# Kernel tuning notes

Measured on AMD Instinct MI355X. Metric: run time of the kernel, lower is better.

The kernel has to match this reference:

```python
import jax, jax.numpy as jnp
import numpy as np

EPS = 1e-8


def box2corners(box):
    # box: (B,N,5) = x,y,w,h,alpha -> corners (B,N,4,2), CCW template
    x, y, w, h, alpha = (box[..., i] for i in range(5))
    tx = jnp.array([0.5, -0.5, -0.5, 0.5], dtype=box.dtype)
    ty = jnp.array([0.5, 0.5, -0.5, -0.5], dtype=box.dtype)
    x_off = w[..., None] * tx          # (B,N,4)
    y_off = h[..., None] * ty
    c = jnp.cos(alpha)[..., None]
    s = jnp.sin(alpha)[..., None]
    cx = x[..., None] + c * x_off - s * y_off
    cy = y[..., None] + s * x_off + c * y_off
    return jnp.stack([cx, cy], axis=-1)


def box_intersection(corners1, corners2):
    # all pairwise edge intersections: (B,N,4,4,2) points + (B,N,4,4) mask
    line1 = jnp.concatenate([corners1, jnp.roll(corners1, -1, axis=2)], axis=-1)
    line2 = jnp.concatenate([corners2, jnp.roll(corners2, -1, axis=2)], axis=-1)
    l1 = line1[:, :, :, None, :]   # (B,N,4,1,4)
    l2 = line2[:, :, None, :, :]   # (B,N,1,4,4)
    x1, y1, x2, y2 = (l1[..., i] for i in range(4))
    x3, y3, x4, y4 = (l2[..., i] for i in range(4))
    num = (y4 - y3) * (x2 - x1) - (x4 - x3) * (y2 - y1)
    den_t = (x4 - x3) * (y1 - y3) - (y4 - y3) * (x1 - x3)
    den_u = (x2 - x1) * (y1 - y3) - (y2 - y1) * (x1 - x3)
    safe = jnp.where(num == 0., 1., num)
    t = jnp.where(num == 0., -1., den_t / safe)
    u = jnp.where(num == 0., -1., -den_u / safe)
    mask = (t > 0.) & (t < 1.) & (u > 0.) & (u < 1.)
    px = x1 + t * (x2 - x1)
    py = y1 + t * (y2 - y1)
    pts = jnp.stack([px, py], axis=-1) * mask[..., None].astype(corners1.dtype)
    return pts, mask


def box1_in_box2(corners1, corners2):
    # which corners of box1 lie inside box2 -> (B,N,4) bool
    a = corners2[:, :, 0:1, :]
    b = corners2[:, :, 1:2, :]
    d = corners2[:, :, 3:4, :]
    ab, ad, am = b - a, d - a, corners1 - a
    p_ab = jnp.sum(ab * am, axis=-1)
    p_ad = jnp.sum(ad * am, axis=-1)
    n_ab = jnp.sum(ab * ab, axis=-1)
    n_ad = jnp.sum(ad * ad, axis=-1)
    eps = 1e-6
    c1 = (p_ab / n_ab > -eps) & (p_ab / n_ab < 1. + eps)
    c2 = (p_ad / n_ad > -eps) & (p_ad / n_ad < 1. + eps)
    return c1 & c2


def oriented_box_intersection_2d(corners1, corners2):
    # intersection area of two rotated boxes via vertex sort + shoelace
    inters, m_int = box_intersection(corners1, corners2)       # (B,N,4,4,2)
    c1_in_2 = box1_in_box2(corners1, corners2)                 # (B,N,4)
    c2_in_1 = box1_in_box2(corners2, corners1)
    B, N = corners1.shape[0], corners1.shape[1]
    verts = jnp.concatenate([corners1, corners2,
                             inters.reshape(B, N, 16, 2)], axis=2)  # (B,N,24,2)
    mask = jnp.concatenate([c1_in_2, c2_in_1,
                            m_int.reshape(B, N, 16)], axis=2)       # (B,N,24)
    maskf = mask.astype(verts.dtype)
    nv = jnp.sum(mask, axis=-1)                                # (B,N) int, num valid
    mean = (jnp.sum(verts * maskf[..., None], axis=2, keepdims=True)
            / jnp.maximum(nv[..., None, None].astype(verts.dtype), 1.))
    rel = verts - mean
    ang = jnp.where(mask, jnp.arctan2(rel[..., 1], rel[..., 0]), 1e6)
    order = jnp.argsort(ang, axis=-1)                          # valid CCW, invalid last
    sorted_v = jnp.take_along_axis(verts, order[..., None], axis=2)
    # pad invalid slots with first valid vertex: zero shoelace contribution
    sel = jnp.arange(24)[None, None, :] < nv[..., None]
    poly = jnp.where(sel[..., None], sorted_v, sorted_v[:, :, 0:1, :])
    nxt = jnp.roll(poly, -1, axis=2)
    area = 0.5 * jnp.abs(jnp.sum(poly[..., 0] * nxt[..., 1]
                                 - nxt[..., 0] * poly[..., 1], axis=-1))
    return area


def diff_iou_rotated_3d(box3d1, box3d2):
    # boxes: (B,N,7) = x,y,z,dx,dy,dz,yaw
    idx = jnp.array([0, 1, 3, 4, 6])
    c1 = box2corners(box3d1[..., idx])
    c2 = box2corners(box3d2[..., idx])
    inter_2d = oriented_box_intersection_2d(c1, c2)
    zmax1 = box3d1[..., 2] + box3d1[..., 5] * 0.5
    zmin1 = box3d1[..., 2] - box3d1[..., 5] * 0.5
    zmax2 = box3d2[..., 2] + box3d2[..., 5] * 0.5
    zmin2 = box3d2[..., 2] - box3d2[..., 5] * 0.5
    z_overlap = jnp.clip(jnp.minimum(zmax1, zmax2) - jnp.maximum(zmin1, zmin2), 0.)
    inter_3d = inter_2d * z_overlap
    v1 = box3d1[..., 3] * box3d1[..., 4] * box3d1[..., 5]
    v2 = box3d2[..., 3] * box3d2[..., 4] * box3d2[..., 5]
    union = v1 + v2 - inter_3d
    return inter_3d / union


def setup_inputs() -> dict:
    key = jax.random.key(0)
    k1, k2, k3, k4, k5 = jax.random.split(key, 5)
    N = 500000
    ctr = jax.random.uniform(k1, (N, 3), minval=-40., maxval=40.)
    dims = jax.random.uniform(k2, (N, 3), minval=1., maxval=5.)
    yaw = jax.random.uniform(k3, (N, 1), minval=-np.pi, maxval=np.pi)
    pred = jnp.concatenate([ctr, dims, yaw], axis=-1).astype(jnp.float32)
    noise = jax.random.normal(k4, (N, 7), dtype=jnp.float32) * jnp.array(
        [0.5, 0.5, 0.3, 0.3, 0.3, 0.3, 0.2], dtype=jnp.float32)
    target = pred + noise
    target = target.at[:, 3:6].set(jnp.maximum(target[:, 3:6], 0.5))
    weight = jax.random.uniform(k5, (N,), dtype=jnp.float32)
    return {"pred": pred, "target": target, "weight": weight}


def reference(pred, target, weight):
    loss_weight = 1.0
    target = jnp.where(jnp.isnan(target), pred, target)
    iou = diff_iou_rotated_3d(pred[None], target[None])        # (1,N)
    loss = 1. - iou
    loss = loss * weight[None]
    return loss_weight * jnp.mean(loss)
```

## Files before the change

### kernel.cpp

```cpp
#include <hip/hip_runtime.h>
#include <hip/hip_fp16.h>
#include <math.h>

#define THREADS 64
#define VSTRIDE 25

__device__ __forceinline__ float prcp(float x) { return __builtin_amdgcn_rcpf(x); }

__device__ __forceinline__ unsigned packh2(float x, float y) {
    __half2 h = __floats2half2_rn(x, y);
    return *reinterpret_cast<unsigned*>(&h);
}
__device__ __forceinline__ void unpackh2(unsigned u, float& x, float& y) {
    __half2 h = *reinterpret_cast<__half2*>(&u);
    x = __low2float(h); y = __high2float(h);
}

__global__ void __launch_bounds__(THREADS) iou3d_kernel(
    const float* __restrict__ pred, const float* __restrict__ tgt,
    const float* __restrict__ wgt, float* __restrict__ partial, int N) {
    __shared__ unsigned ldsbuf[THREADS * VSTRIDE];
    int tid = threadIdx.x;
    unsigned* myv = &ldsbuf[tid * VSTRIDE];
    int n = blockIdx.x * THREADS + tid;
    float loss = 0.0f;
    if (n < N) {
        float p[7], t[7];
#pragma unroll
        for (int k = 0; k < 7; k++) {
            p[k] = pred[(size_t)n * 7 + k];
            float tv = tgt[(size_t)n * 7 + k];
            t[k] = (tv != tv) ? p[k] : tv;
        }
        float w = wgt[n];
        float zmax1 = p[2] + p[5] * 0.5f, zmin1 = p[2] - p[5] * 0.5f;
        float zmax2 = t[2] + t[5] * 0.5f, zmin2 = t[2] - t[5] * 0.5f;
        float zov = fmaxf(fminf(zmax1, zmax2) - fmaxf(zmin1, zmin2), 0.0f);
        float vol1 = p[3] * p[4] * p[5], vol2 = t[3] * t[4] * t[5];

        float hw1 = 0.5f * p[3], hh1 = 0.5f * p[4];
        float hw2 = 0.5f * t[3], hh2 = 0.5f * t[4];
        float s1, c1v, s2, c2v;
        __sincosf(p[6], &s1, &c1v);
        __sincosf(t[6], &s2, &c2v);
        float c12 = c1v * c2v + s1 * s2;
        float s12 = s1 * c2v - c1v * s2;
        float ddx = p[0] - t[0], ddy = p[1] - t[1];
        float T12x =  c2v * ddx + s2 * ddy;
        float T12y = -s2 * ddx + c2v * ddy;
        float T21x = -(c1v * ddx + s1 * ddy);
        float T21y =  s1 * ddx - c1v * ddy;
        float ux = c12 * hw1, uy = s12 * hw1;
        float wx = -s12 * hh1, wy = c12 * hh1;
        float fx[4], fy[4];
        fx[0] = T12x + ux + wx; fy[0] = T12y + uy + wy;
        fx[1] = T12x - ux + wx; fy[1] = T12y - uy + wy;
        fx[2] = T12x - ux - wx; fy[2] = T12y - uy - wy;
        fx[3] = T12x + ux - wx; fy[3] = T12y + uy - wy;

        unsigned vm = 0;
        float bx2 = hw2 * (1.0f + 2e-6f), by2 = hh2 * (1.0f + 2e-6f);
#pragma unroll
        for (int k = 0; k < 4; k++) {
            bool c = (fabsf(fx[k]) < bx2) && (fabsf(fy[k]) < by2);
            vm |= ((unsigned)c) << k;
        }
        float u2x = c12 * hw2, u2y = -s12 * hw2;
        float v2x = s12 * hh2, v2y = c12 * hh2;
        float bx1 = hw1 * (1.0f + 2e-6f), by1 = hh1 * (1.0f + 2e-6f);
        {
            float qx, qy;
            qx = T21x + u2x + v2x; qy = T21y + u2y + v2y;
            vm |= ((unsigned)((fabsf(qx) < bx1) && (fabsf(qy) < by1))) << 4;
            qx = T21x - u2x + v2x; qy = T21y - u2y + v2y;
            vm |= ((unsigned)((fabsf(qx) < bx1) && (fabsf(qy) < by1))) << 5;
            qx = T21x - u2x - v2x; qy = T21y - u2y - v2y;
            vm |= ((unsigned)((fabsf(qx) < bx1) && (fabsf(qy) < by1))) << 6;
            qx = T21x + u2x - v2x; qy = T21y + u2y - v2y;
            vm |= ((unsigned)((fabsf(qx) < bx1) && (fabsf(qy) < by1))) << 7;
        }
        float sx = 0.0f, sy = 0.0f;
#pragma unroll
        for (int k = 0; k < 4; k++) {
            myv[k] = packh2(fx[k], fy[k]);
            bool v = (vm >> k) & 1u;
            sx += v ? fx[k] : 0.0f; sy += v ? fy[k] : 0.0f;
        }
        myv[4] = packh2(hw2, hh2);  myv[5] = packh2(-hw2, hh2);
        myv[6] = packh2(-hw2, -hh2); myv[7] = packh2(hw2, -hh2);
        {
            bool v4 = (vm >> 4) & 1u, v5 = (vm >> 5) & 1u, v6 = (vm >> 6) & 1u, v7 = (vm >> 7) & 1u;
            sx += (v4 ? hw2 : 0.0f) + (v5 ? -hw2 : 0.0f) + (v6 ? -hw2 : 0.0f) + (v7 ? hw2 : 0.0f);
            sy += (v4 ? hh2 : 0.0f) + (v5 ? hh2 : 0.0f) + (v6 ? -hh2 : 0.0f) + (v7 ? -hh2 : 0.0f);
        }

        float tux = ux + ux, tuy = uy + uy, twx = wx + wx, twy = wy + wy;
        float rtux = prcp(tux), rtuy = prcp(tuy), rtwx = prcp(twx), rtwy = prcp(twy);
        float dxe[4] = {-tux, -twx, tux, twx};
        float dye[4] = {-tuy, -twy, tuy, twy};
        float rdxe[4] = {-rtux, -rtwx, rtux, rtwx};
        float rdye[4] = {-rtuy, -rtwy, rtuy, rtwy};
        float r2w = prcp(hw2 + hw2), r2h = prcp(hh2 + hh2);

        float pvar[16];
#pragma unroll
        for (int e1 = 0; e1 < 4; e1++) {
            float x1 = fx[e1], y1 = fy[e1];
            {
                float tt = (hh2 - y1) * rdye[e1];
                float px = fmaf(tt, dxe[e1], x1);
                float uu = (hw2 - px) * (-r2w);
                bool mk = (tt > 0.0f) && (tt < 1.0f) && (uu > 0.0f) && (uu < 1.0f);
                pvar[e1 * 4 + 0] = px;
                float pxm = mk ? px : 0.0f, pym = mk ? hh2 : 0.0f;
                myv[8 + e1 * 4 + 0] = packh2(pxm, pym);
                sx += pxm; sy += pym;
                vm |= ((unsigned)mk) << (8 + e1 * 4 + 0);
            }
            {
                float tt = (-hw2 - x1) * rdxe[e1];
                float py = fmaf(tt, dye[e1], y1);
                float uu = (hh2 - py) * (-r2h);
                bool mk = (tt > 0.0f) && (tt < 1.0f) && (uu > 0.0f) && (uu < 1.0f);
                pvar[e1 * 4 + 1] = py;
                float pxm = mk ? -hw2 : 0.0f, pym = mk ? py : 0.0f;
                myv[8 + e1 * 4 + 1] = packh2(pxm, pym);
                sx += pxm; sy += pym;
                vm |= ((unsigned)mk) << (8 + e1 * 4 + 1);
            }
            {
                float tt = (-hh2 - y1) * rdye[e1];
                float px = fmaf(tt, dxe[e1], x1);
                float uu = (-hw2 - px) * r2w;
                bool mk = (tt > 0.0f) && (tt < 1.0f) && (uu > 0.0f) && (uu < 1.0f);
                pvar[e1 * 4 + 2] = px;
                float pxm = mk ? px : 0.0f, pym = mk ? -hh2 : 0.0f;
                myv[8 + e1 * 4 + 2] = packh2(pxm, pym);
                sx += pxm; sy += pym;
                vm |= ((unsigned)mk) << (8 + e1 * 4 + 2);
            }
            {
                float tt = (hw2 - x1) * rdxe[e1];
                float py = fmaf(tt, dye[e1], y1);
                float uu = (-hh2 - py) * r2h;
                bool mk = (tt > 0.0f) && (tt < 1.0f) && (uu > 0.0f) && (uu < 1.0f);
                pvar[e1 * 4 + 3] = py;
                float pxm = mk ? hw2 : 0.0f, pym = mk ? py : 0.0f;
                myv[8 + e1 * 4 + 3] = packh2(pxm, pym);
                sx += pxm; sy += pym;
                vm |= ((unsigned)mk) << (8 + e1 * 4 + 3);
            }
        }

        int nv = __popc(vm);
        float r0 = prcp(fmaxf((float)nv, 1.0f));
        float mx = sx * r0, my = sy * r0;

        unsigned ka[24];
#define MKKEY(K, XR, YR) do { \
        float xr_ = (XR), yr_ = (YR); \
        float d_ = fabsf(xr_) + fabsf(yr_); \
        float q_ = 1.0f - xr_ * prcp(d_); \
        float pa_ = copysignf(q_, yr_) + 4.0f; \
        unsigned key_ = (__float_as_uint(pa_) & 0xFFFFFFE0u) | (unsigned)(K); \
        ka[K] = ((vm >> (K)) & 1u) ? key_ : (0x7F000000u | (unsigned)(K)); \
    } while (0)
        float hpx = hw2 - mx, hmx = -hw2 - mx, hpy = hh2 - my, hmy = -hh2 - my;
#pragma unroll
        for (int k = 0; k < 4; k++) MKKEY(k, fx[k] - mx, fy[k] - my);
        MKKEY(4, hpx, hpy); MKKEY(5, hmx, hpy); MKKEY(6, hmx, hmy); MKKEY(7, hpx, hmy);
#pragma unroll
        for (int e1 = 0; e1 < 4; e1++) {
            MKKEY(8 + e1 * 4 + 0, pvar[e1 * 4 + 0] - mx, hpy);
            MKKEY(8 + e1 * 4 + 1, hmx, pvar[e1 * 4 + 1] - my);
            MKKEY(8 + e1 * 4 + 2, pvar[e1 * 4 + 2] - mx, hmy);
            MKKEY(8 + e1 * 4 + 3, hpx, pvar[e1 * 4 + 3] - my);
        }
#undef MKKEY

#define CE(A, B) { unsigned lo_ = ka[A] < ka[B] ? ka[A] : ka[B]; \
                   unsigned hi_ = ka[A] < ka[B] ? ka[B] : ka[A]; \
                   ka[A] = lo_; ka[B] = hi_; }
        CE(0,1); CE(2,3); CE(4,5); CE(6,7); CE(8,9); CE(10,11); CE(12,13); CE(14,15); CE(16,17); CE(18,19); CE(20,21); CE(22,23);
        CE(0,2); CE(1,3); CE(4,6); CE(5,7); CE(8,10); CE(9,11); CE(12,14); CE(13,15); CE(16,18); CE(17,19); CE(20,22); CE(21,23);
        CE(1,2); CE(5,6); CE(9,10); CE(13,14); CE(17,18); CE(21,22);
        CE(0,4); CE(1,5); CE(2,6); CE(3,7); CE(8,12); CE(9,13); CE(10,14); CE(11,15); CE(16,20); CE(17,21); CE(18,22); CE(19,23);
        CE(2,4); CE(3,5); CE(10,12); CE(11,13); CE(18,20); CE(19,21);
        CE(1,2); CE(3,4); CE(5,6); CE(9,10); CE(11,12); CE(13,14); CE(17,18); CE(19,20); CE(21,22);
        CE(0,8); CE(1,9); CE(2,10); CE(3,11); CE(4,12); CE(5,13); CE(6,14); CE(7,15);
        CE(4,8); CE(5,9); CE(6,10); CE(7,11);
        CE(2,4); CE(3,5); CE(6,8); CE(7,9); CE(10,12); CE(11,13); CE(18,20); CE(19,21);
        CE(1,2); CE(3,4); CE(5,6); CE(7,8); CE(9,10); CE(11,12); CE(13,14); CE(17,18); CE(19,20); CE(21,22);
        CE(0,16); CE(1,17); CE(2,18); CE(3,19); CE(4,20); CE(5,21); CE(6,22); CE(7,23);
        CE(8,16); CE(9,17); CE(10,18); CE(11,19); CE(12,20); CE(13,21); CE(14,22); CE(15,23);
        CE(4,8); CE(5,9); CE(6,10); CE(7,11); CE(12,16); CE(13,17); CE(14,18); CE(15,19);
        CE(2,4); CE(3,5); CE(6,8); CE(7,9); CE(10,12); CE(11,13); CE(14,16); CE(15,17); CE(18,20); CE(19,21);
        CE(1,2); CE(3,4); CE(5,6); CE(7,8); CE(9,10); CE(11,12); CE(13,14); CE(15,16); CE(17,18); CE(19,20); CE(21,22);
#undef CE

        unsigned gu[24];
#pragma unroll
        for (int i = 0; i < 24; i++) gu[i] = myv[ka[i] & 31u];
        float g0x, g0y;
        unpackh2(gu[0], g0x, g0y);
        float prevx = g0x, prevy = g0y;
        float area2 = 0.0f;
#pragma unroll
        for (int i = 1; i < 24; i++) {
            float xx, yy;
            unpackh2(gu[i], xx, yy);
            bool c = i < nv;
            float cxv = c ? xx : g0x;
            float cyv = c ? yy : g0y;
            area2 += prevx * cyv - cxv * prevy;
            prevx = cxv; prevy = cyv;
        }
        area2 += prevx * g0y - g0x * prevy;
        float inter2d = 0.5f * fabsf(area2);

        float inter3d = inter2d * zov;
        float uni = vol1 + vol2 - inter3d;
        float iou = inter3d / uni;
        loss = (1.0f - iou) * w;
    }

#pragma unroll
    for (int off = 32; off > 0; off >>= 1) loss += __shfl_down(loss, off, 64);
    if (threadIdx.x == 0) partial[blockIdx.x] = loss;
}

__global__ void __launch_bounds__(1024) reduce_kernel(const float* __restrict__ partial,
                                                      int nb, float* __restrict__ out, int N) {
    float s = 0.0f;
    for (int i = threadIdx.x; i < nb; i += 1024) s += partial[i];
#pragma unroll
    for (int off = 32; off > 0; off >>= 1) s += __shfl_down(s, off, 64);
    __shared__ float sm[16];
    int lane = threadIdx.x & 63, wv = threadIdx.x >> 6;
    if (lane == 0) sm[wv] = s;
    __syncthreads();
    if (threadIdx.x == 0) {
        float tot = 0.0f;
#pragma unroll
        for (int k = 0; k < 16; k++) tot += sm[k];
        out[0] = tot / (float)N;
    }
}

extern "C" void kernel_launch(void* const* d_in, const int* in_sizes, int n_in,
                              void* d_out, int out_size, void* d_ws, size_t ws_size,
                              hipStream_t stream) {
    const float* pred = (const float*)d_in[0];
    const float* tgt  = (const float*)d_in[1];
    const float* wgt  = (const float*)d_in[2];
    int N = in_sizes[2];
    int nb = (N + THREADS - 1) / THREADS;
    float* partial = (float*)d_ws;
    iou3d_kernel<<<nb, THREADS, 0, stream>>>(pred, tgt, wgt, partial, N);
    reduce_kernel<<<1, 1024, 0, stream>>>(partial, nb, (float*)d_out, N);
}
```

Measured before the change: 28.76 us.

## Process two boxes per thread with interleaved sorting networks and column-major LDS

Each thread now handles two box pairs and interleaves their 24-key sorting networks, giving the scheduler independent instructions to hide latency. The LDS vertex buffer is changed from a per-thread stride of 25 to a slot-major layout indexed by thread id, which changes the bank access pattern. The edge-intersection range test now compares the intersection coordinate against multiples of the half extents instead of multiplying by precomputed reciprocals, dropping two rcp operations. Register pressure roughly doubles and the grid is halved, which may reduce occupancy and the number of waves in flight.

```diff
diff --git a/kernel.cpp b/kernel.cpp
--- a/kernel.cpp
+++ b/kernel.cpp
@@ -3,7 +3,6 @@
 #include <math.h>
 
 #define THREADS 64
-#define VSTRIDE 25
 
 __device__ __forceinline__ float prcp(float x) { return __builtin_amdgcn_rcpf(x); }
 
@@ -19,27 +18,41 @@
 __global__ void __launch_bounds__(THREADS) iou3d_kernel(
     const float* __restrict__ pred, const float* __restrict__ tgt,
     const float* __restrict__ wgt, float* __restrict__ partial, int N) {
-    __shared__ unsigned ldsbuf[THREADS * VSTRIDE];
+    __shared__ unsigned ldsbuf[48 * THREADS];
     int tid = threadIdx.x;
-    unsigned* myv = &ldsbuf[tid * VSTRIDE];
-    int n = blockIdx.x * THREADS + tid;
+#define LDSV(Q, S) ldsbuf[((((Q) * 24) + (S)) << 6) + tid]
     float loss = 0.0f;
-    if (n < N) {
+
+    float zov[2], volsum[2], wgtv[2], hw2a[2], hh2a[2];
+    float fxa[2][4], fya[2][4];
+    float pv[2][16];
+    float sxa[2], sya[2];
+    unsigned vma[2];
+    int nva[2];
+    unsigned ka0[24], ka1[24];
+
+#pragma unroll
+    for (int q = 0; q < 2; q++) {
+        int n = blockIdx.x * (2 * THREADS) + tid + q * THREADS;
+        bool live = n < N;
+        int nc = live ? n : (N - 1);
         float p[7], t[7];
 #pragma unroll
         for (int k = 0; k < 7; k++) {
-            p[k] = pred[(size_t)n * 7 + k];
-            float tv = tgt[(size_t)n * 7 + k];
+            p[k] = pred[(size_t)nc * 7 + k];
+            float tv = tgt[(size_t)nc * 7 + k];
             t[k] = (tv != tv) ? p[k] : tv;
         }
-        float w = wgt[n];
+        wgtv[q] = live ? wgt[nc] : 0.0f;
+
         float zmax1 = p[2] + p[5] * 0.5f, zmin1 = p[2] - p[5] * 0.5f;
         float zmax2 = t[2] + t[5] * 0.5f, zmin2 = t[2] - t[5] * 0.5f;
-        float zov = fmaxf(fminf(zmax1, zmax2) - fmaxf(zmin1, zmin2), 0.0f);
-        float vol1 = p[3] * p[4] * p[5], vol2 = t[3] * t[4] * t[5];
+        zov[q] = fmaxf(fminf(zmax1, zmax2) - fmaxf(zmin1, zmin2), 0.0f);
+        volsum[q] = p[3] * p[4] * p[5] + t[3] * t[4] * t[5];
 
         float hw1 = 0.5f * p[3], hh1 = 0.5f * p[4];
         float hw2 = 0.5f * t[3], hh2 = 0.5f * t[4];
+        hw2a[q] = hw2; hh2a[q] = hh2;
         float s1, c1v, s2, c2v;
         __sincosf(p[6], &s1, &c1v);
         __sincosf(t[6], &s2, &c2v);
@@ -57,6 +70,8 @@
         fx[1] = T12x - ux + wx; fy[1] = T12y - uy + wy;
         fx[2] = T12x - ux - wx; fy[2] = T12y - uy - wy;
         fx[3] = T12x + ux - wx; fy[3] = T12y + uy - wy;
+#pragma unroll
+        for (int k = 0; k < 4; k++) { fxa[q][k] = fx[k]; fya[q][k] = fy[k]; }
 
         unsigned vm = 0;
         float bx2 = hw2 * (1.0f + 2e-6f), by2 = hh2 * (1.0f + 2e-6f);
@@ -82,12 +97,12 @@
         float sx = 0.0f, sy = 0.0f;
 #pragma unroll
         for (int k = 0; k < 4; k++) {
-            myv[k] = packh2(fx[k], fy[k]);
+            LDSV(q, k) = packh2(fx[k], fy[k]);
             bool v = (vm >> k) & 1u;
             sx += v ? fx[k] : 0.0f; sy += v ? fy[k] : 0.0f;
         }
-        myv[4] = packh2(hw2, hh2);  myv[5] = packh2(-hw2, hh2);
-        myv[6] = packh2(-hw2, -hh2); myv[7] = packh2(hw2, -hh2);
+        LDSV(q, 4) = packh2(hw2, hh2);   LDSV(q, 5) = packh2(-hw2, hh2);
+        LDSV(q, 6) = packh2(-hw2, -hh2); LDSV(q, 7) = packh2(hw2, -hh2);
         {
             bool v4 = (vm >> 4) & 1u, v5 = (vm >> 5) & 1u, v6 = (vm >> 6) & 1u, v7 = (vm >> 7) & 1u;
             sx += (v4 ? hw2 : 0.0f) + (v5 ? -hw2 : 0.0f) + (v6 ? -hw2 : 0.0f) + (v7 ? hw2 : 0.0f);
@@ -100,129 +115,138 @@
         float dye[4] = {-tuy, -twy, tuy, twy};
         float rdxe[4] = {-rtux, -rtwx, rtux, rtwx};
         float rdye[4] = {-rtuy, -rtwy, rtuy, rtwy};
-        float r2w = prcp(hw2 + hw2), r2h = prcp(hh2 + hh2);
-
-        float pvar[16];
+        float w3 = 3.0f * hw2, h3 = 3.0f * hh2;
 #pragma unroll
         for (int e1 = 0; e1 < 4; e1++) {
             float x1 = fx[e1], y1 = fy[e1];
             {
                 float tt = (hh2 - y1) * rdye[e1];
                 float px = fmaf(tt, dxe[e1], x1);
-                float uu = (hw2 - px) * (-r2w);
-                bool mk = (tt > 0.0f) && (tt < 1.0f) && (uu > 0.0f) && (uu < 1.0f);
-                pvar[e1 * 4 + 0] = px;
+                bool mk = (tt > 0.0f) && (tt < 1.0f) && (px > hw2) && (px < w3);
+                pv[q][e1 * 4 + 0] = px;
                 float pxm = mk ? px : 0.0f, pym = mk ? hh2 : 0.0f;
-                myv[8 + e1 * 4 + 0] = packh2(pxm, pym);
+                LDSV(q, 8 + e1 * 4 + 0) = packh2(pxm, pym);
                 sx += pxm; sy += pym;
                 vm |= ((unsigned)mk) << (8 + e1 * 4 + 0);
             }
             {
                 float tt = (-hw2 - x1) * rdxe[e1];
                 float py = fmaf(tt, dye[e1], y1);
-                float uu = (hh2 - py) * (-r2h);
-                bool mk = (tt > 0.0f) && (tt < 1.0f) && (uu > 0.0f) && (uu < 1.0f);
-                pvar[e1 * 4 + 1] = py;
+                bool mk = (tt > 0.0f) && (tt < 1.0f) && (py > hh2) && (py < h3);
+                pv[q][e1 * 4 + 1] = py;
                 float pxm = mk ? -hw2 : 0.0f, pym = mk ? py : 0.0f;
-                myv[8 + e1 * 4 + 1] = packh2(pxm, pym);
+                LDSV(q, 8 + e1 * 4 + 1) = packh2(pxm, pym);
                 sx += pxm; sy += pym;
                 vm |= ((unsigned)mk) << (8 + e1 * 4 + 1);
             }
             {
                 float tt = (-hh2 - y1) * rdye[e1];
                 float px = fmaf(tt, dxe[e1], x1);
-                float uu = (-hw2 - px) * r2w;
-                bool mk = (tt > 0.0f) && (tt < 1.0f) && (uu > 0.0f) && (uu < 1.0f);
-                pvar[e1 * 4 + 2] = px;
+                bool mk = (tt > 0.0f) && (tt < 1.0f) && (px < -hw2) && (px > -w3);
+                pv[q][e1 * 4 + 2] = px;
                 float pxm = mk ? px : 0.0f, pym = mk ? -hh2 : 0.0f;
-                myv[8 + e1 * 4 + 2] = packh2(pxm, pym);
+                LDSV(q, 8 + e1 * 4 + 2) = packh2(pxm, pym);
                 sx += pxm; sy += pym;
                 vm |= ((unsigned)mk) << (8 + e1 * 4 + 2);
             }
             {
                 float tt = (hw2 - x1) * rdxe[e1];
                 float py = fmaf(tt, dye[e1], y1);
-                float uu = (-hh2 - py) * r2h;
-                bool mk = (tt > 0.0f) && (tt < 1.0f) && (uu > 0.0f) && (uu < 1.0f);
-                pvar[e1 * 4 + 3] = py;
+                bool mk = (tt > 0.0f) && (tt < 1.0f) && (py < -hh2) && (py > -h3);
+                pv[q][e1 * 4 + 3] = py;
                 float pxm = mk ? hw2 : 0.0f, pym = mk ? py : 0.0f;
-                myv[8 + e1 * 4 + 3] = packh2(pxm, pym);
+                LDSV(q, 8 + e1 * 4 + 3) = packh2(pxm, pym);
                 sx += pxm; sy += pym;
                 vm |= ((unsigned)mk) << (8 + e1 * 4 + 3);
             }
         }
-
-        int nv = __popc(vm);
-        float r0 = prcp(fmaxf((float)nv, 1.0f));
-        float mx = sx * r0, my = sy * r0;
-
-        unsigned ka[24];
-#define MKKEY(K, XR, YR) do { \
+        vma[q] = vm; sxa[q] = sx; sya[q] = sy;
+    }
+
+#define KEYBUILD(Q, KA) do { \
+        unsigned vm = vma[Q]; \
+        int nv = __popc(vm); nva[Q] = nv; \
+        float r0 = prcp(fmaxf((float)nv, 1.0f)); \
+        float mx = sxa[Q] * r0, my = sya[Q] * r0; \
+        float hw2 = hw2a[Q], hh2 = hh2a[Q]; \
+        float hpx = hw2 - mx, hmx = -hw2 - mx, hpy = hh2 - my, hmy = -hh2 - my; \
+        MK(KA, 0, fxa[Q][0] - mx, fya[Q][0] - my); \
+        MK(KA, 1, fxa[Q][1] - mx, fya[Q][1] - my); \
+        MK(KA, 2, fxa[Q][2] - mx, fya[Q][2] - my); \
+        MK(KA, 3, fxa[Q][3] - mx, fya[Q][3] - my); \
+        MK(KA, 4, hpx, hpy); MK(KA, 5, hmx, hpy); MK(KA, 6, hmx, hmy); MK(KA, 7, hpx, hmy); \
+        MK(KA, 8,  pv[Q][0] - mx, hpy);  MK(KA, 9,  hmx, pv[Q][1] - my); \
+        MK(KA, 10, pv[Q][2] - mx, hmy);  MK(KA, 11, hpx, pv[Q][3] - my); \
+        MK(KA, 12, pv[Q][4] - mx, hpy);  MK(KA, 13, hmx, pv[Q][5] - my); \
+        MK(KA, 14, pv[Q][6] - mx, hmy);  MK(KA, 15, hpx, pv[Q][7] - my); \
+        MK(KA, 16, pv[Q][8] - mx, hpy);  MK(KA, 17, hmx, pv[Q][9] - my); \
+        MK(KA, 18, pv[Q][10] - mx, hmy); MK(KA, 19, hpx, pv[Q][11] - my); \
+        MK(KA, 20, pv[Q][12] - mx, hpy); MK(KA, 21, hmx, pv[Q][13] - my); \
+        MK(KA, 22, pv[Q][14] - mx, hmy); MK(KA, 23, hpx, pv[Q][15] - my); \
+    } while (0)
+#define MK(KA, K, XR, YR) do { \
         float xr_ = (XR), yr_ = (YR); \
         float d_ = fabsf(xr_) + fabsf(yr_); \
         float q_ = 1.0f - xr_ * prcp(d_); \
         float pa_ = copysignf(q_, yr_) + 4.0f; \
         unsigned key_ = (__float_as_uint(pa_) & 0xFFFFFFE0u) | (unsigned)(K); \
-        ka[K] = ((vm >> (K)) & 1u) ? key_ : (0x7F000000u | (unsigned)(K)); \
+        KA[K] = ((vm >> (K)) & 1u) ? key_ : (0x7F000000u | (unsigned)(K)); \
     } while (0)
-        float hpx = hw2 - mx, hmx = -hw2 - mx, hpy = hh2 - my, hmy = -hh2 - my;
-#pragma unroll
-        for (int k = 0; k < 4; k++) MKKEY(k, fx[k] - mx, fy[k] - my);
-        MKKEY(4, hpx, hpy); MKKEY(5, hmx, hpy); MKKEY(6, hmx, hmy); MKKEY(7, hpx, hmy);
-#pragma unroll
-        for (int e1 = 0; e1 < 4; e1++) {
-            MKKEY(8 + e1 * 4 + 0, pvar[e1 * 4 + 0] - mx, hpy);
-            MKKEY(8 + e1 * 4 + 1, hmx, pvar[e1 * 4 + 1] - my);
-            MKKEY(8 + e1 * 4 + 2, pvar[e1 * 4 + 2] - mx, hmy);
-            MKKEY(8 + e1 * 4 + 3, hpx, pvar[e1 * 4 + 3] - my);
-        }
-#undef MKKEY
-
-#define CE(A, B) { unsigned lo_ = ka[A] < ka[B] ? ka[A] : ka[B]; \
-                   unsigned hi_ = ka[A] < ka[B] ? ka[B] : ka[A]; \
-                   ka[A] = lo_; ka[B] = hi_; }
-        CE(0,1); CE(2,3); CE(4,5); CE(6,7); CE(8,9); CE(10,11); CE(12,13); CE(14,15); CE(16,17); CE(18,19); CE(20,21); CE(22,23);
-        CE(0,2); CE(1,3); CE(4,6); CE(5,7); CE(8,10); CE(9,11); CE(12,14); CE(13,15); CE(16,18); CE(17,19); CE(20,22); CE(21,23);
-        CE(1,2); CE(5,6); CE(9,10); CE(13,14); CE(17,18); CE(21,22);
-        CE(0,4); CE(1,5); CE(2,6); CE(3,7); CE(8,12); CE(9,13); CE(10,14); CE(11,15); CE(16,20); CE(17,21); CE(18,22); CE(19,23);
-        CE(2,4); CE(3,5); CE(10,12); CE(11,13); CE(18,20); CE(19,21);
-        CE(1,2); CE(3,4); CE(5,6); CE(9,10); CE(11,12); CE(13,14); CE(17,18); CE(19,20); CE(21,22);
-        CE(0,8); CE(1,9); CE(2,10); CE(3,11); CE(4,12); CE(5,13); CE(6,14); CE(7,15);
-        CE(4,8); CE(5,9); CE(6,10); CE(7,11);
-        CE(2,4); CE(3,5); CE(6,8); CE(7,9); CE(10,12); CE(11,13); CE(18,20); CE(19,21);
-        CE(1,2); CE(3,4); CE(5,6); CE(7,8); CE(9,10); CE(11,12); CE(13,14); CE(17,18); CE(19,20); CE(21,22);
-        CE(0,16); CE(1,17); CE(2,18); CE(3,19); CE(4,20); CE(5,21); CE(6,22); CE(7,23);
-        CE(8,16); CE(9,17); CE(10,18); CE(11,19); CE(12,20); CE(13,21); CE(14,22); CE(15,23);
-        CE(4,8); CE(5,9); CE(6,10); CE(7,11); CE(12,16); CE(13,17); CE(14,18); CE(15,19);
-        CE(2,4); CE(3,5); CE(6,8); CE(7,9); CE(10,12); CE(11,13); CE(14,16); CE(15,17); CE(18,20); CE(19,21);
-        CE(1,2); CE(3,4); CE(5,6); CE(7,8); CE(9,10); CE(11,12); CE(13,14); CE(15,16); CE(17,18); CE(19,20); CE(21,22);
+    KEYBUILD(0, ka0);
+    KEYBUILD(1, ka1);
+#undef MK
+#undef KEYBUILD
+
+#define CE1(KA, A, B) { unsigned lo_ = KA[A] < KA[B] ? KA[A] : KA[B]; \
+                        unsigned hi_ = KA[A] < KA[B] ? KA[B] : KA[A]; \
+                        KA[A] = lo_; KA[B] = hi_; }
+#define CE(A, B) CE1(ka0, A, B) CE1(ka1, A, B)
+    CE(0,1); CE(2,3); CE(4,5); CE(6,7); CE(8,9); CE(10,11); CE(12,13); CE(14,15); CE(16,17); CE(18,19); CE(20,21); CE(22,23);
+    CE(0,2); CE(1,3); CE(4,6); CE(5,7); CE(8,10); CE(9,11); CE(12,14); CE(13,15); CE(16,18); CE(17,19); CE(20,22); CE(21,23);
+    CE(1,2); CE(5,6); CE(9,10); CE(13,14); CE(17,18); CE(21,22);
+    CE(0,4); CE(1,5); CE(2,6); CE(3,7); CE(8,12); CE(9,13); CE(10,14); CE(11,15); CE(16,20); CE(17,21); CE(18,22); CE(19,23);
+    CE(2,4); CE(3,5); CE(10,12); CE(11,13); CE(18,20); CE(19,21);
+    CE(1,2); CE(3,4); CE(5,6); CE(9,10); CE(11,12); CE(13,14); CE(17,18); CE(19,20); CE(21,22);
+    CE(0,8); CE(1,9); CE(2,10); CE(3,11); CE(4,12); CE(5,13); CE(6,14); CE(7,15);
+    CE(4,8); CE(5,9); CE(6,10); CE(7,11);
+    CE(2,4); CE(3,5); CE(6,8); CE(7,9); CE(10,12); CE(11,13); CE(18,20); CE(19,21);
+    CE(1,2); CE(3,4); CE(5,6); CE(7,8); CE(9,10); CE(11,12); CE(13,14); CE(17,18); CE(19,20); CE(21,22);
+    CE(0,16); CE(1,17); CE(2,18); CE(3,19); CE(4,20); CE(5,21); CE(6,22); CE(7,23);
+    CE(8,16); CE(9,17); CE(10,18); CE(11,19); CE(12,20); CE(13,21); CE(14,22); CE(15,23);
+    CE(4,8); CE(5,9); CE(6,10); CE(7,11); CE(12,16); CE(13,17); CE(14,18); CE(15,19);
+    CE(2,4); CE(3,5); CE(6,8); CE(7,9); CE(10,12); CE(11,13); CE(14,16); CE(15,17); CE(18,20); CE(19,21);
+    CE(1,2); CE(3,4); CE(5,6); CE(7,8); CE(9,10); CE(11,12); CE(13,14); CE(15,16); CE(17,18); CE(19,20); CE(21,22);
 #undef CE
-
-        unsigned gu[24];
-#pragma unroll
-        for (int i = 0; i < 24; i++) gu[i] = myv[ka[i] & 31u];
-        float g0x, g0y;
-        unpackh2(gu[0], g0x, g0y);
-        float prevx = g0x, prevy = g0y;
-        float area2 = 0.0f;
-#pragma unroll
-        for (int i = 1; i < 24; i++) {
-            float xx, yy;
-            unpackh2(gu[i], xx, yy);
-            bool c = i < nv;
-            float cxv = c ? xx : g0x;
-            float cyv = c ? yy : g0y;
-            area2 += prevx * cyv - cxv * prevy;
-            prevx = cxv; prevy = cyv;
-        }
-        area2 += prevx * g0y - g0x * prevy;
-        float inter2d = 0.5f * fabsf(area2);
-
-        float inter3d = inter2d * zov;
-        float uni = vol1 + vol2 - inter3d;
-        float iou = inter3d / uni;
-        loss = (1.0f - iou) * w;
-    }
+#undef CE1
+
+#define SHOELACE(Q, KA) do { \
+        unsigned gu[24]; \
+        _Pragma("unroll") \
+        for (int i = 0; i < 24; i++) \
+            gu[i] = ldsbuf[((((Q) * 24) + (KA[i] & 31u)) << 6) + tid]; \
+        int nv = nva[Q]; \
+        float g0x, g0y; unpackh2(gu[0], g0x, g0y); \
+        float prevx = g0x, prevy = g0y, area2 = 0.0f; \
+        _Pragma("unroll") \
+        for (int i = 1; i < 24; i++) { \
+            float xx, yy; unpackh2(gu[i], xx, yy); \
+            bool c = i < nv; \
+            float cxv = c ? xx : g0x; \
+            float cyv = c ? yy : g0y; \
+            area2 += prevx * cyv - cxv * prevy; \
+            prevx = cxv; prevy = cyv; \
+        } \
+        area2 += prevx * g0y - g0x * prevy; \
+        float inter2d = 0.5f * fabsf(area2); \
+        float inter3d = inter2d * zov[Q]; \
+        float uni = volsum[Q] - inter3d; \
+        float iou = inter3d / uni; \
+        loss += (1.0f - iou) * wgtv[Q]; \
+    } while (0)
+    SHOELACE(0, ka0);
+    SHOELACE(1, ka1);
+#undef SHOELACE
+#undef LDSV
 
 #pragma unroll
     for (int off = 32; off > 0; off >>= 1) loss += __shfl_down(loss, off, 64);
@@ -254,7 +278,7 @@
     const float* tgt  = (const float*)d_in[1];
     const float* wgt  = (const float*)d_in[2];
     int N = in_sizes[2];
-    int nb = (N + THREADS - 1) / THREADS;
+    int nb = (N + 2 * THREADS - 1) / (2 * THREADS);
     float* partial = (float*)d_ws;
     iou3d_kernel<<<nb, THREADS, 0, stream>>>(pred, tgt, wgt, partial, N);
     reduce_kernel<<<1, 1024, 0, stream>>>(partial, nb, (float*)d_out, N);
```

Result: no change. 28.57 us (-0.7%).
